# Performance work log

Measured on AMD Instinct MI355X. Metric: run time of the kernel, lower is better.

Reference implementation:

```python
import jax, jax.numpy as jnp
import numpy as np

B, T, C = 2, 2048, 1024
H, DK, OUT = 16, 64, 1024


def setup_inputs() -> dict:
    key = jax.random.key(0)
    k1, k2, k3, k4, k5 = jax.random.split(key, 5)
    glorot_qkv = (2.0 / (C + H * DK)) ** 0.5  # glorot_normal stddev for [C,H,DK]
    glorot_o = (2.0 / (H * DK + OUT)) ** 0.5
    return {
        "x": jax.random.normal(k1, (B, T, C), dtype=jnp.float32),
        "query_mat": jax.random.normal(k2, (C, H, DK), dtype=jnp.float32) * glorot_qkv,
        "key_mat": jax.random.normal(k3, (C, H, DK), dtype=jnp.float32) * glorot_qkv,
        "value_mat": jax.random.normal(k4, (C, H, DK), dtype=jnp.float32) * glorot_qkv,
        "linear_m1": jax.random.normal(k5, (H * DK, OUT), dtype=jnp.float32) * glorot_o,
    }


def reference(x, query_mat, key_mat, value_mat, linear_m1):
    # x: [B,T,C]; projections: [C,H,DK]
    q = jnp.einsum('btc,chd->bhtd', x, query_mat)
    k = jnp.einsum('btc,chd->bhtd', x, key_mat)
    v = jnp.einsum('btc,chd->bhtd', x, value_mat)
    d_k = query_mat.shape[-1]
    # NOTE: faithful to source, which MULTIPLIES by sqrt(d_k)
    w = jnp.einsum('bhtd,bhzd->bhtz', q, k) * (d_k ** 0.5)
    t = w.shape[-1]
    causal = jnp.tril(jnp.ones((t, t), dtype=bool))  # [T,T]
    w = jnp.where(causal, w, -jnp.inf)
    w = jax.nn.softmax(w, axis=-1)
    # dropout inactive (training=False)
    o = jnp.einsum('bhtz,bhzd->bhtd', w, v)
    o = o.transpose(0, 2, 1, 3).reshape(o.shape[0], o.shape[2], -1)  # [B,T,H*DK]
    return jnp.einsum('btc,cz->btz', o, linear_m1)
```

## Files before the change

kernel.cpp:

```cpp
#include <hip/hip_runtime.h>


typedef unsigned short u16;
typedef unsigned int u32;
typedef unsigned long long u64;
typedef __attribute__((ext_vector_type(8))) short bf16x8;
typedef __attribute__((ext_vector_type(4))) float f32x4;

__device__ inline u16 f2bf(float f) {
  union { float f; unsigned u; } v; v.f = f;
  unsigned r = v.u + 0x7FFFu + ((v.u >> 16) & 1u);
  return (u16)(r >> 16);
}
__device__ inline float bf2f(u16 h) {
  union { unsigned u; float f; } v; v.u = ((unsigned)h) << 16;
  return v.f;
}
__device__ inline void glds16(const u16* g, u16* s) {
  __builtin_amdgcn_global_load_lds(
      (const __attribute__((address_space(1))) u32*)g,
      (__attribute__((address_space(3))) u32*)s, 16, 0, 0);
}
#define MFMA __builtin_amdgcn_mfma_f32_16x16x32_bf16
#define SP(P) __builtin_amdgcn_s_setprio(P)

__global__ __launch_bounds__(256) void prep(
    const float* __restrict__ x,
    const float* __restrict__ wq, const float* __restrict__ wk,
    const float* __restrict__ wv, const float* __restrict__ wo,
    u16* __restrict__ Xh, u16* __restrict__ Xl,
    u16* __restrict__ Wqh, u16* __restrict__ Wql,
    u16* __restrict__ Wkh, u16* __restrict__ Wkl,
    u16* __restrict__ Wvt, u16* __restrict__ Wot) {
  const int z = blockIdx.z;
  const int tid = threadIdx.x;
  if (z == 0) {
    const int bid = blockIdx.y * 32 + blockIdx.x;
#pragma unroll
    for (int k = 0; k < 4; k++) {
      int i = bid * 4096 + k * 1024 + tid * 4;
      float4 v = *(const float4*)(x + i);
      ushort4 h, l;
      h.x = f2bf(v.x); l.x = f2bf(v.x - bf2f(h.x));
      h.y = f2bf(v.y); l.y = f2bf(v.y - bf2f(h.y));
      h.z = f2bf(v.z); l.z = f2bf(v.z - bf2f(h.z));
      h.w = f2bf(v.w); l.w = f2bf(v.w - bf2f(h.w));
      *(ushort4*)(Xh + i) = h;
      *(ushort4*)(Xl + i) = l;
    }
    return;
  }
  __shared__ float tile[32][33];
  const float* W = (z == 1) ? wq : (z == 2) ? wk : (z == 3) ? wv : wo;
  const int bx = blockIdx.x * 32, by = blockIdx.y * 32;
  const int tx = tid & 31, ty = tid >> 5;
#pragma unroll
  for (int j = 0; j < 32; j += 8)
    tile[ty + j][tx] = W[(size_t)(by + ty + j) * 1024 + bx + tx];
  __syncthreads();
  if (z <= 2) {
    u16* Th = (z == 1) ? Wqh : Wkh;
    u16* Tl = (z == 1) ? Wql : Wkl;
#pragma unroll
    for (int j = 0; j < 32; j += 8) {
      float v = tile[tx][ty + j];
      u16 h = f2bf(v);
      size_t idx = (size_t)(bx + ty + j) * 1024 + by + tx;
      Th[idx] = h;
      Tl[idx] = f2bf(v - bf2f(h));
    }
  } else {
    u16* T = (z == 3) ? Wvt : Wot;
#pragma unroll
    for (int j = 0; j < 32; j += 8)
      T[(size_t)(bx + ty + j) * 1024 + by + tx] = f2bf(tile[tx][ty + j]);
  }
}

__global__ __launch_bounds__(256) void gemm_qkv(
    const u16* __restrict__ Xh, const u16* __restrict__ Xl,
    const u16* __restrict__ Wqh, const u16* __restrict__ Wql,
    const u16* __restrict__ Wkh, const u16* __restrict__ Wkl,
    const u16* __restrict__ Wvt,
    u16* __restrict__ Qh, u16* __restrict__ Ql,
    u16* __restrict__ Kh, u16* __restrict__ Kl,
    u16* __restrict__ Vt) {
  __shared__ u16 S[4][128][32];
  const int K = 1024;
  const int z = blockIdx.z;
  const bool split = (z < 2);
  const u16* Bh = (z == 0) ? Wqh : (z == 1) ? Wkh : Wvt;
  const u16* Bl = (z == 0) ? Wql : Wkl;
  const int tid = threadIdx.x;
  const int lane = tid & 63, wv = tid >> 6;
  const int quad = lane >> 4, lc = lane & 15;
  const int m0 = (blockIdx.x * 4 + (blockIdx.y & 3)) * 128;
  const int n0 = (blockIdx.y >> 2) * 128;
  const int wm = (wv >> 1) * 64, wn = (wv & 1) * 64;
  const int lrow = lane >> 2, lk = (lane & 3) * 8;
  const u16* a0p = Xh + (size_t)(m0 + wv * 32 + lrow) * K + lk;
  const u16* a1p = a0p + 16 * K;
  const u16* al0p = Xl + (size_t)(m0 + wv * 32 + lrow) * K + lk;
  const u16* al1p = al0p + 16 * K;
  const u16* b0p = Bh + (size_t)(n0 + wv * 32 + lrow) * K + lk;
  const u16* b1p = b0p + 16 * K;
  const u16* bl0p = split ? (Bl + (size_t)(n0 + wv * 32 + lrow) * K + lk) : b0p;
  const u16* bl1p = bl0p + 16 * K;
  u16* sA0 = &S[0][wv * 32][0];      u16* sA1 = &S[0][wv * 32 + 16][0];
  u16* sAl0 = &S[1][wv * 32][0];     u16* sAl1 = &S[1][wv * 32 + 16][0];
  u16* sB0 = &S[2][wv * 32][0];      u16* sB1 = &S[2][wv * 32 + 16][0];
  u16* sBl0 = &S[3][wv * 32][0];     u16* sBl1 = &S[3][wv * 32 + 16][0];
  f32x4 acc[4][4];
#pragma unroll
  for (int i = 0; i < 4; i++)
#pragma unroll
    for (int j = 0; j < 4; j++) acc[i][j] = (f32x4){0.f, 0.f, 0.f, 0.f};
  for (int kc = 0; kc < K; kc += 32) {
    __syncthreads();
    glds16(a0p + kc, sA0); glds16(a1p + kc, sA1);
    glds16(b0p + kc, sB0); glds16(b1p + kc, sB1);
    if (split) {
      glds16(al0p + kc, sAl0); glds16(al1p + kc, sAl1);
      glds16(bl0p + kc, sBl0); glds16(bl1p + kc, sBl1);
    }
    __syncthreads();
    bf16x8 ah[4], al[4];
#pragma unroll
    for (int mt = 0; mt < 4; mt++)
      ah[mt] = *(const bf16x8*)&S[0][wm + mt * 16 + lc][quad * 8];
    if (split) {
#pragma unroll
      for (int mt = 0; mt < 4; mt++)
        al[mt] = *(const bf16x8*)&S[1][wm + mt * 16 + lc][quad * 8];
    }
#pragma unroll
    for (int nt = 0; nt < 4; nt++) {
      bf16x8 bfh = *(const bf16x8*)&S[2][wn + nt * 16 + lc][quad * 8];
#pragma unroll
      for (int mt = 0; mt < 4; mt++)
        acc[mt][nt] = MFMA(ah[mt], bfh, acc[mt][nt], 0, 0, 0);
      if (split) {
        bf16x8 bfl = *(const bf16x8*)&S[3][wn + nt * 16 + lc][quad * 8];
#pragma unroll
        for (int mt = 0; mt < 4; mt++) {
          acc[mt][nt] = MFMA(ah[mt], bfl, acc[mt][nt], 0, 0, 0);
          acc[mt][nt] = MFMA(al[mt], bfh, acc[mt][nt], 0, 0, 0);
        }
      }
    }
  }
  const int rb = quad * 4;
  if (z == 2) {
#pragma unroll
    for (int mt = 0; mt < 4; mt++)
#pragma unroll
      for (int nt = 0; nt < 4; nt++)
#pragma unroll
        for (int r = 0; r < 4; r++) {
          int m = m0 + wm + mt * 16 + rb + r, n = n0 + wn + nt * 16 + lc;
          int b = m >> 11, t = m & 2047, h = n >> 6, d = n & 63;
          Vt[((size_t)(b * 16 + h) * 64 + d) * 2048 + t] = f2bf(acc[mt][nt][r]);
        }
  } else {
    u16* Ch = (z == 0) ? Qh : Kh;
    u16* Cl = (z == 0) ? Ql : Kl;
    const float scale = (z == 0) ? 11.541560327111707f : 1.0f;
#pragma unroll
    for (int mt = 0; mt < 4; mt++)
#pragma unroll
      for (int nt = 0; nt < 4; nt++)
#pragma unroll
        for (int r = 0; r < 4; r++) {
          int m = m0 + wm + mt * 16 + rb + r, n = n0 + wn + nt * 16 + lc;
          int b = m >> 11, t = m & 2047, h = n >> 6, d = n & 63;
          float v = acc[mt][nt][r] * scale;
          u16 hv = f2bf(v);
          size_t idx = ((size_t)(b * 16 + h) * 2048 + t) * 64 + d;
          Ch[idx] = hv;
          Cl[idx] = f2bf(v - bf2f(hv));
        }
  }
}

__global__ __launch_bounds__(256) void gemm_out(const u16* __restrict__ A,
                                                const u16* __restrict__ Bt,
                                                float* __restrict__ C) {
  __shared__ u16 Sa[64][32], Sb[128][32];
  const int K = 1024, N = 1024;
  const int tid = threadIdx.x;
  const int lane = tid & 63, wv = tid >> 6;
  const int quad = lane >> 4, lc = lane & 15;
  const int m0 = (blockIdx.x * 8 + (blockIdx.y & 7)) * 64;
  const int n0 = (blockIdx.y >> 3) * 128;
  const int wm = (wv >> 1) * 32, wn = (wv & 1) * 64;
  const int lrow = lane >> 2, lk = (lane & 3) * 8;
  const u16* ap = A + (size_t)(m0 + wv * 16 + lrow) * K + lk;
  const u16* b0p = Bt + (size_t)(n0 + wv * 32 + lrow) * K + lk;
  const u16* b1p = b0p + 16 * K;
  u16* sA = &Sa[wv * 16][0];
  u16* sB0 = &Sb[wv * 32][0];
  u16* sB1 = &Sb[wv * 32 + 16][0];
  f32x4 acc[2][4];
#pragma unroll
  for (int i = 0; i < 2; i++)
#pragma unroll
    for (int j = 0; j < 4; j++) acc[i][j] = (f32x4){0.f, 0.f, 0.f, 0.f};
  for (int kc = 0; kc < K; kc += 32) {
    __syncthreads();
    glds16(ap + kc, sA);
    glds16(b0p + kc, sB0);
    glds16(b1p + kc, sB1);
    __syncthreads();
    bf16x8 ah[2];
#pragma unroll
    for (int mt = 0; mt < 2; mt++)
      ah[mt] = *(const bf16x8*)&Sa[wm + mt * 16 + lc][quad * 8];
#pragma unroll
    for (int nt = 0; nt < 4; nt++) {
      bf16x8 bfh = *(const bf16x8*)&Sb[wn + nt * 16 + lc][quad * 8];
#pragma unroll
      for (int mt = 0; mt < 2; mt++)
        acc[mt][nt] = MFMA(ah[mt], bfh, acc[mt][nt], 0, 0, 0);
    }
  }
#pragma unroll
  for (int mt = 0; mt < 2; mt++)
#pragma unroll
    for (int nt = 0; nt < 4; nt++)
#pragma unroll
      for (int r = 0; r < 4; r++)
        C[(size_t)(m0 + wm + mt * 16 + quad * 4 + r) * N + n0 + wn + nt * 16 + lc] =
            acc[mt][nt][r];
}

__global__ __launch_bounds__(256, 2) void attn(const u16* __restrict__ Qh,
                                               const u16* __restrict__ Ql,
                                               const u16* __restrict__ Kh,
                                               const u16* __restrict__ Kl,
                                               const u16* __restrict__ Vt,
                                               u16* __restrict__ O16) {
  __shared__ u16 Khs[2][64][64], Kls[2][64][64], Vs[2][64][64];
  __shared__ u16 Ps[4][16][72];
  const int tid = threadIdx.x;
  const int lane = tid & 63, w = tid >> 6;
  const int quad = lane >> 4, lc = lane & 15;
  const int i = blockIdx.x;
  const int bh = i & 31;
  const int qb = 31 - (i >> 5);
  const int ng = qb + 1;
  const int tq = qb * 64 + w * 16 + lc;
  const size_t kbase = (size_t)bh * 2048 * 64;
  const size_t vbase = (size_t)bh * 64 * 2048;
  const size_t qoff = kbase + (size_t)tq * 64 + quad * 8;
  bf16x8 qh0 = *(const bf16x8*)(Qh + qoff);
  bf16x8 qh1 = *(const bf16x8*)(Qh + qoff + 32);
  bf16x8 ql0 = *(const bf16x8*)(Ql + qoff);
  bf16x8 ql1 = *(const bf16x8*)(Ql + qoff + 32);
  const int srow = lane >> 3;
  const int scol = (lane & 7) ^ srow;
  const u16* kg0 = Kh + kbase + (size_t)(w * 16 + srow) * 64 + scol * 8;
  const u16* lg0 = Kl + kbase + (size_t)(w * 16 + srow) * 64 + scol * 8;
  const u16* vg0 = Vt + vbase + (size_t)(w * 16 + srow) * 2048 + scol * 8;

  float mi = -3.0e38f, li = 0.f;
  f32x4 o[4];
#pragma unroll
  for (int d = 0; d < 4; d++) o[d] = (f32x4){0.f, 0.f, 0.f, 0.f};
  const int rx = lc & 7;

  {
    glds16(kg0, &Khs[0][w * 16][0]); glds16(kg0 + 8 * 64, &Khs[0][w * 16 + 8][0]);
    glds16(lg0, &Kls[0][w * 16][0]); glds16(lg0 + 8 * 64, &Kls[0][w * 16 + 8][0]);
    glds16(vg0, &Vs[0][w * 16][0]);  glds16(vg0 + 8 * 2048, &Vs[0][w * 16 + 8][0]);
  }
  for (int g = 0; g < ng; g++) {
    const int buf = g & 1;
    const int z0 = g * 64;
    __syncthreads();
    if (g + 1 < ng) {
      const int zn = (g + 1) * 64;
      const int nb = buf ^ 1;
      glds16(kg0 + (size_t)zn * 64, &Khs[nb][w * 16][0]);
      glds16(kg0 + (size_t)zn * 64 + 8 * 64, &Khs[nb][w * 16 + 8][0]);
      glds16(lg0 + (size_t)zn * 64, &Kls[nb][w * 16][0]);
      glds16(lg0 + (size_t)zn * 64 + 8 * 64, &Kls[nb][w * 16 + 8][0]);
      glds16(vg0 + zn, &Vs[nb][w * 16][0]);
      glds16(vg0 + zn + 8 * 2048, &Vs[nb][w * 16 + 8][0]);
    }
    f32x4 s[4];
    SP(1);
#pragma unroll
    for (int tt = 0; tt < 4; tt++) {
      const int R = tt * 16 + lc;
      bf16x8 kh0 = *(const bf16x8*)&Khs[buf][R][(quad ^ rx) * 8];
      bf16x8 kh1 = *(const bf16x8*)&Khs[buf][R][((4 + quad) ^ rx) * 8];
      bf16x8 kl0 = *(const bf16x8*)&Kls[buf][R][(quad ^ rx) * 8];
      bf16x8 kl1 = *(const bf16x8*)&Kls[buf][R][((4 + quad) ^ rx) * 8];
      f32x4 sv = (f32x4){0.f, 0.f, 0.f, 0.f};
      sv = MFMA(kh0, qh0, sv, 0, 0, 0);
      sv = MFMA(kh1, qh1, sv, 0, 0, 0);
      sv = MFMA(kh0, ql0, sv, 0, 0, 0);
      sv = MFMA(kh1, ql1, sv, 0, 0, 0);
      sv = MFMA(kl0, qh0, sv, 0, 0, 0);
      sv = MFMA(kl1, qh1, sv, 0, 0, 0);
      s[tt] = sv;
    }
    SP(0);
    if (g == ng - 1) {
#pragma unroll
      for (int tt = 0; tt < 4; tt++)
#pragma unroll
        for (int r = 0; r < 4; r++)
          if (z0 + tt * 16 + quad * 4 + r > tq) s[tt][r] = -3.0e38f;
    }
    float smax = -3.0e38f;
#pragma unroll
    for (int tt = 0; tt < 4; tt++)
#pragma unroll
      for (int r = 0; r < 4; r++) smax = fmaxf(smax, s[tt][r]);
    smax = fmaxf(smax, __shfl_xor(smax, 16));
    smax = fmaxf(smax, __shfl_xor(smax, 32));
    if (!__all(smax - mi <= 8.0f)) {
      float mnew = fmaxf(mi, smax);
      float alpha = __builtin_amdgcn_exp2f(mi - mnew);
      mi = mnew;
      li *= alpha;
#pragma unroll
      for (int d = 0; d < 4; d++) o[d] *= alpha;
    }
    float rs = 0.f;
#pragma unroll
    for (int tt = 0; tt < 4; tt++) {
      union { u16 h[4]; u64 d; } pk;
#pragma unroll
      for (int r = 0; r < 4; r++) {
        float p = __builtin_amdgcn_exp2f(s[tt][r] - mi);
        rs += p;
        pk.h[r] = f2bf(p);
      }
      *(u64*)&Ps[w][lc][tt * 16 + quad * 4] = pk.d;
    }
    li += rs;
    bf16x8 pf0 = *(const bf16x8*)&Ps[w][lc][quad * 8];
    bf16x8 pf1 = *(const bf16x8*)&Ps[w][lc][32 + quad * 8];
    SP(1);
#pragma unroll
    for (int dd = 0; dd < 4; dd++) {
      const int R = dd * 16 + lc;
      bf16x8 va0 = *(const bf16x8*)&Vs[buf][R][(quad ^ rx) * 8];
      bf16x8 va1 = *(const bf16x8*)&Vs[buf][R][((4 + quad) ^ rx) * 8];
      o[dd] = MFMA(va0, pf0, o[dd], 0, 0, 0);
      o[dd] = MFMA(va1, pf1, o[dd], 0, 0, 0);
    }
    SP(0);
  }
  li += __shfl_xor(li, 16);
  li += __shfl_xor(li, 32);
  const float rli = 1.0f / li;
  const int b = bh >> 4, hh = bh & 15;
  const size_t obase = ((size_t)(b * 2048 + tq)) * 1024 + hh * 64 + quad * 4;
#pragma unroll
  for (int dd = 0; dd < 4; dd++) {
    ushort4 ov;
    ov.x = f2bf(o[dd][0] * rli);
    ov.y = f2bf(o[dd][1] * rli);
    ov.z = f2bf(o[dd][2] * rli);
    ov.w = f2bf(o[dd][3] * rli);
    *(ushort4*)&O16[obase + dd * 16] = ov;
  }
}

extern "C" void kernel_launch(void* const* d_in, const int* in_sizes, int n_in,
                              void* d_out, int out_size, void* d_ws, size_t ws_size,
                              hipStream_t stream) {
  const float* x  = (const float*)d_in[0];
  const float* wq = (const float*)d_in[1];
  const float* wk = (const float*)d_in[2];
  const float* wv = (const float*)d_in[3];
  const float* wo = (const float*)d_in[4];

  char* w = (char*)d_ws;
  const size_t MB = 1u << 20;
  u16* Xh  = (u16*)(w + 0 * MB);
  u16* Xl  = (u16*)(w + 8 * MB);
  u16* Wqh = (u16*)(w + 16 * MB);
  u16* Wql = (u16*)(w + 18 * MB);
  u16* Wkh = (u16*)(w + 20 * MB);
  u16* Wkl = (u16*)(w + 22 * MB);
  u16* Wvt = (u16*)(w + 24 * MB);
  u16* Wot = (u16*)(w + 26 * MB);
  u16* Qhb = (u16*)(w + 28 * MB);
  u16* Qlb = (u16*)(w + 36 * MB);
  u16* Khb = (u16*)(w + 44 * MB);
  u16* Klb = (u16*)(w + 52 * MB);
  u16* Vtb = (u16*)(w + 60 * MB);
  u16* O16 = (u16*)(w + 0 * MB);

  hipLaunchKernelGGL(prep, dim3(32, 32, 5), dim3(256), 0, stream,
                     x, wq, wk, wv, wo, Xh, Xl, Wqh, Wql, Wkh, Wkl, Wvt, Wot);

  hipLaunchKernelGGL(gemm_qkv, dim3(8, 32, 3), dim3(256), 0, stream,
                     Xh, Xl, Wqh, Wql, Wkh, Wkl, Wvt, Qhb, Qlb, Khb, Klb, Vtb);

  hipLaunchKernelGGL(attn, dim3(1024), dim3(256), 0, stream,
                     Qhb, Qlb, Khb, Klb, Vtb, O16);

  hipLaunchKernelGGL(gemm_out, dim3(8, 64), dim3(256), 0, stream, O16, Wot, (float*)d_out);
}
```

Measured before the change: 214.5 us.

## Load K low-part directly to registers, drop its LDS buffer, raise occupancy

```diff
diff --git a/kernel.cpp b/kernel.cpp
--- a/kernel.cpp
+++ b/kernel.cpp
@@ -233,13 +233,13 @@
             acc[mt][nt][r];
 }
 
-__global__ __launch_bounds__(256, 2) void attn(const u16* __restrict__ Qh,
+__global__ __launch_bounds__(256, 3) void attn(const u16* __restrict__ Qh,
                                                const u16* __restrict__ Ql,
                                                const u16* __restrict__ Kh,
                                                const u16* __restrict__ Kl,
                                                const u16* __restrict__ Vt,
                                                u16* __restrict__ O16) {
-  __shared__ u16 Khs[2][64][64], Kls[2][64][64], Vs[2][64][64];
+  __shared__ u16 Khs[2][64][64], Vs[2][64][64];
   __shared__ u16 Ps[4][16][72];
   const int tid = threadIdx.x;
   const int lane = tid & 63, w = tid >> 6;
@@ -259,8 +259,8 @@
   const int srow = lane >> 3;
   const int scol = (lane & 7) ^ srow;
   const u16* kg0 = Kh + kbase + (size_t)(w * 16 + srow) * 64 + scol * 8;
-  const u16* lg0 = Kl + kbase + (size_t)(w * 16 + srow) * 64 + scol * 8;
   const u16* vg0 = Vt + vbase + (size_t)(w * 16 + srow) * 2048 + scol * 8;
+  const u16* klp = Kl + kbase + (size_t)lc * 64 + quad * 8;
 
   float mi = -3.0e38f, li = 0.f;
   f32x4 o[4];
@@ -268,92 +268,93 @@
   for (int d = 0; d < 4; d++) o[d] = (f32x4){0.f, 0.f, 0.f, 0.f};
   const int rx = lc & 7;
 
-  {
-    glds16(kg0, &Khs[0][w * 16][0]); glds16(kg0 + 8 * 64, &Khs[0][w * 16 + 8][0]);
-    glds16(lg0, &Kls[0][w * 16][0]); glds16(lg0 + 8 * 64, &Kls[0][w * 16 + 8][0]);
-    glds16(vg0, &Vs[0][w * 16][0]);  glds16(vg0 + 8 * 2048, &Vs[0][w * 16 + 8][0]);
-  }
-  for (int g = 0; g < ng; g++) {
-    const int buf = g & 1;
-    const int z0 = g * 64;
-    __syncthreads();
-    if (g + 1 < ng) {
-      const int zn = (g + 1) * 64;
-      const int nb = buf ^ 1;
-      glds16(kg0 + (size_t)zn * 64, &Khs[nb][w * 16][0]);
-      glds16(kg0 + (size_t)zn * 64 + 8 * 64, &Khs[nb][w * 16 + 8][0]);
-      glds16(lg0 + (size_t)zn * 64, &Kls[nb][w * 16][0]);
-      glds16(lg0 + (size_t)zn * 64 + 8 * 64, &Kls[nb][w * 16 + 8][0]);
-      glds16(vg0 + zn, &Vs[nb][w * 16][0]);
-      glds16(vg0 + zn + 8 * 2048, &Vs[nb][w * 16 + 8][0]);
-    }
-    f32x4 s[4];
-    SP(1);
-#pragma unroll
-    for (int tt = 0; tt < 4; tt++) {
-      const int R = tt * 16 + lc;
-      bf16x8 kh0 = *(const bf16x8*)&Khs[buf][R][(quad ^ rx) * 8];
-      bf16x8 kh1 = *(const bf16x8*)&Khs[buf][R][((4 + quad) ^ rx) * 8];
-      bf16x8 kl0 = *(const bf16x8*)&Kls[buf][R][(quad ^ rx) * 8];
-      bf16x8 kl1 = *(const bf16x8*)&Kls[buf][R][((4 + quad) ^ rx) * 8];
-      f32x4 sv = (f32x4){0.f, 0.f, 0.f, 0.f};
-      sv = MFMA(kh0, qh0, sv, 0, 0, 0);
-      sv = MFMA(kh1, qh1, sv, 0, 0, 0);
-      sv = MFMA(kh0, ql0, sv, 0, 0, 0);
-      sv = MFMA(kh1, ql1, sv, 0, 0, 0);
-      sv = MFMA(kl0, qh0, sv, 0, 0, 0);
-      sv = MFMA(kl1, qh1, sv, 0, 0, 0);
-      s[tt] = sv;
-    }
-    SP(0);
-    if (g == ng - 1) {
-#pragma unroll
-      for (int tt = 0; tt < 4; tt++)
-#pragma unroll
-        for (int r = 0; r < 4; r++)
-          if (z0 + tt * 16 + quad * 4 + r > tq) s[tt][r] = -3.0e38f;
-    }
-    float smax = -3.0e38f;
-#pragma unroll
-    for (int tt = 0; tt < 4; tt++)
-#pragma unroll
-      for (int r = 0; r < 4; r++) smax = fmaxf(smax, s[tt][r]);
-    smax = fmaxf(smax, __shfl_xor(smax, 16));
-    smax = fmaxf(smax, __shfl_xor(smax, 32));
-    if (!__all(smax - mi <= 8.0f)) {
-      float mnew = fmaxf(mi, smax);
-      float alpha = __builtin_amdgcn_exp2f(mi - mnew);
-      mi = mnew;
-      li *= alpha;
-#pragma unroll
-      for (int d = 0; d < 4; d++) o[d] *= alpha;
-    }
-    float rs = 0.f;
-#pragma unroll
-    for (int tt = 0; tt < 4; tt++) {
-      union { u16 h[4]; u64 d; } pk;
-#pragma unroll
-      for (int r = 0; r < 4; r++) {
-        float p = __builtin_amdgcn_exp2f(s[tt][r] - mi);
-        rs += p;
-        pk.h[r] = f2bf(p);
-      }
-      *(u64*)&Ps[w][lc][tt * 16 + quad * 4] = pk.d;
-    }
-    li += rs;
-    bf16x8 pf0 = *(const bf16x8*)&Ps[w][lc][quad * 8];
-    bf16x8 pf1 = *(const bf16x8*)&Ps[w][lc][32 + quad * 8];
-    SP(1);
-#pragma unroll
-    for (int dd = 0; dd < 4; dd++) {
-      const int R = dd * 16 + lc;
-      bf16x8 va0 = *(const bf16x8*)&Vs[buf][R][(quad ^ rx) * 8];
-      bf16x8 va1 = *(const bf16x8*)&Vs[buf][R][((4 + quad) ^ rx) * 8];
-      o[dd] = MFMA(va0, pf0, o[dd], 0, 0, 0);
-      o[dd] = MFMA(va1, pf1, o[dd], 0, 0, 0);
-    }
-    SP(0);
-  }
+  bf16x8 kA0[4], kA1[4], kB0[4], kB1[4];
+#define LOAD_KL(D0, D1, G) do { const u16* kg_ = klp + (size_t)(G) * 4096; \
+    _Pragma("unroll") for (int tt = 0; tt < 4; tt++) { \
+      D0[tt] = *(const bf16x8*)(kg_ + tt * 1024); \
+      D1[tt] = *(const bf16x8*)(kg_ + tt * 1024 + 32); } } while (0)
+
+  glds16(kg0, &Khs[0][w * 16][0]); glds16(kg0 + 8 * 64, &Khs[0][w * 16 + 8][0]);
+  glds16(vg0, &Vs[0][w * 16][0]);  glds16(vg0 + 8 * 2048, &Vs[0][w * 16 + 8][0]);
+  LOAD_KL(kA0, kA1, 0);
+
+#define BODY(G, CUR0, CUR1, NXT0, NXT1) do { \
+    const int buf = (G) & 1; \
+    const int z0 = (G) * 64; \
+    __syncthreads();  \
+    if ((G) + 1 < ng) { \
+      const int zn = ((G) + 1) * 64; \
+      const int nb = buf ^ 1; \
+      glds16(kg0 + (size_t)zn * 64, &Khs[nb][w * 16][0]); \
+      glds16(kg0 + (size_t)zn * 64 + 8 * 64, &Khs[nb][w * 16 + 8][0]); \
+      glds16(vg0 + zn, &Vs[nb][w * 16][0]); \
+      glds16(vg0 + zn + 8 * 2048, &Vs[nb][w * 16 + 8][0]); \
+      LOAD_KL(NXT0, NXT1, (G) + 1); \
+    } \
+    f32x4 s[4]; \
+    SP(1); \
+    _Pragma("unroll") for (int tt = 0; tt < 4; tt++) { \
+      const int R = tt * 16 + lc; \
+      bf16x8 kh0 = *(const bf16x8*)&Khs[buf][R][(quad ^ rx) * 8]; \
+      bf16x8 kh1 = *(const bf16x8*)&Khs[buf][R][((4 + quad) ^ rx) * 8]; \
+      f32x4 sv = (f32x4){0.f, 0.f, 0.f, 0.f}; \
+      sv = MFMA(kh0, qh0, sv, 0, 0, 0); \
+      sv = MFMA(kh1, qh1, sv, 0, 0, 0); \
+      sv = MFMA(kh0, ql0, sv, 0, 0, 0); \
+      sv = MFMA(kh1, ql1, sv, 0, 0, 0); \
+      sv = MFMA(CUR0[tt], qh0, sv, 0, 0, 0); \
+      sv = MFMA(CUR1[tt], qh1, sv, 0, 0, 0); \
+      s[tt] = sv; \
+    } \
+    SP(0); \
+    if ((G) == ng - 1) { \
+      _Pragma("unroll") for (int tt = 0; tt < 4; tt++) \
+        _Pragma("unroll") for (int r = 0; r < 4; r++) \
+          if (z0 + tt * 16 + quad * 4 + r > tq) s[tt][r] = -3.0e38f; \
+    } \
+    float smax = -3.0e38f; \
+    _Pragma("unroll") for (int tt = 0; tt < 4; tt++) \
+      _Pragma("unroll") for (int r = 0; r < 4; r++) smax = fmaxf(smax, s[tt][r]); \
+    smax = fmaxf(smax, __shfl_xor(smax, 16)); \
+    smax = fmaxf(smax, __shfl_xor(smax, 32)); \
+    if (!__all(smax - mi <= 8.0f)) { \
+      float mnew = fmaxf(mi, smax); \
+      float alpha = __builtin_amdgcn_exp2f(mi - mnew); \
+      mi = mnew; \
+      li *= alpha; \
+      _Pragma("unroll") for (int d = 0; d < 4; d++) o[d] *= alpha; \
+    } \
+    float rs = 0.f; \
+    _Pragma("unroll") for (int tt = 0; tt < 4; tt++) { \
+      union { u16 h[4]; u64 d; } pk; \
+      _Pragma("unroll") for (int r = 0; r < 4; r++) { \
+        float p = __builtin_amdgcn_exp2f(s[tt][r] - mi); \
+        rs += p; \
+        pk.h[r] = f2bf(p); \
+      } \
+      *(u64*)&Ps[w][lc][tt * 16 + quad * 4] = pk.d; \
+    } \
+    li += rs; \
+    bf16x8 pf0 = *(const bf16x8*)&Ps[w][lc][quad * 8]; \
+    bf16x8 pf1 = *(const bf16x8*)&Ps[w][lc][32 + quad * 8]; \
+    SP(1); \
+    _Pragma("unroll") for (int dd = 0; dd < 4; dd++) { \
+      const int R = dd * 16 + lc; \
+      bf16x8 va0 = *(const bf16x8*)&Vs[buf][R][(quad ^ rx) * 8]; \
+      bf16x8 va1 = *(const bf16x8*)&Vs[buf][R][((4 + quad) ^ rx) * 8]; \
+      o[dd] = MFMA(va0, pf0, o[dd], 0, 0, 0); \
+      o[dd] = MFMA(va1, pf1, o[dd], 0, 0, 0); \
+    } \
+    SP(0); \
+  } while (0)
+
+  for (int g = 0; g < ng; g += 2) {
+    BODY(g, kA0, kA1, kB0, kB1);
+    if (g + 1 < ng) BODY(g + 1, kB0, kB1, kA0, kA1);
+  }
+#undef BODY
+#undef LOAD_KL
+
   li += __shfl_xor(li, 16);
   li += __shfl_xor(li, 32);
   const float rli = 1.0f / li;
```

Measured after the change: 241.9 us. 12.8% more time.

## Double-buffer output GEMM LDS tiles with 64-wide K steps and prefetch

Applied to the files above, without the earlier changes.

```diff
diff --git a/kernel.cpp b/kernel.cpp
--- a/kernel.cpp
+++ b/kernel.cpp
@@ -185,7 +185,7 @@
 __global__ __launch_bounds__(256) void gemm_out(const u16* __restrict__ A,
                                                 const u16* __restrict__ Bt,
                                                 float* __restrict__ C) {
-  __shared__ u16 Sa[64][32], Sb[128][32];
+  __shared__ u16 Sa[2][64][64], Sb[2][128][64];
   const int K = 1024, N = 1024;
   const int tid = threadIdx.x;
   const int lane = tid & 63, wv = tid >> 6;
@@ -193,36 +193,51 @@
   const int m0 = (blockIdx.x * 8 + (blockIdx.y & 7)) * 64;
   const int n0 = (blockIdx.y >> 3) * 128;
   const int wm = (wv >> 1) * 32, wn = (wv & 1) * 64;
-  const int lrow = lane >> 2, lk = (lane & 3) * 8;
-  const u16* ap = A + (size_t)(m0 + wv * 16 + lrow) * K + lk;
-  const u16* b0p = Bt + (size_t)(n0 + wv * 32 + lrow) * K + lk;
-  const u16* b1p = b0p + 16 * K;
-  u16* sA = &Sa[wv * 16][0];
-  u16* sB0 = &Sb[wv * 32][0];
-  u16* sB1 = &Sb[wv * 32 + 16][0];
+  const int srow = lane >> 3, sck = (lane & 7) * 8;
+  const u16* ap = A + (size_t)(m0 + wv * 16 + srow) * K + sck;
+  const u16* bp = Bt + (size_t)(n0 + wv * 32 + srow) * K + sck;
   f32x4 acc[2][4];
 #pragma unroll
   for (int i = 0; i < 2; i++)
 #pragma unroll
     for (int j = 0; j < 4; j++) acc[i][j] = (f32x4){0.f, 0.f, 0.f, 0.f};
-  for (int kc = 0; kc < K; kc += 32) {
+#define STAGE_OUT(KT, BUF) do { \
+    const u16* a_ = ap + (KT) * 64; \
+    glds16(a_, &Sa[BUF][wv * 16][0]); \
+    glds16(a_ + 8 * K, &Sa[BUF][wv * 16 + 8][0]); \
+    const u16* b_ = bp + (KT) * 64; \
+    glds16(b_, &Sb[BUF][wv * 32][0]); \
+    glds16(b_ + 8 * K, &Sb[BUF][wv * 32 + 8][0]); \
+    glds16(b_ + 16 * K, &Sb[BUF][wv * 32 + 16][0]); \
+    glds16(b_ + 24 * K, &Sb[BUF][wv * 32 + 24][0]); \
+  } while (0)
+  STAGE_OUT(0, 0);
+  for (int kt = 0; kt < 16; kt++) {
+    const int buf = kt & 1;
     __syncthreads();
-    glds16(ap + kc, sA);
-    glds16(b0p + kc, sB0);
-    glds16(b1p + kc, sB1);
-    __syncthreads();
-    bf16x8 ah[2];
+    if (kt + 1 < 16) STAGE_OUT(kt + 1, buf ^ 1);
+    bf16x8 afr[2][2], bfr[4][2];
 #pragma unroll
     for (int mt = 0; mt < 2; mt++)
-      ah[mt] = *(const bf16x8*)&Sa[wm + mt * 16 + lc][quad * 8];
-#pragma unroll
-    for (int nt = 0; nt < 4; nt++) {
-      bf16x8 bfh = *(const bf16x8*)&Sb[wn + nt * 16 + lc][quad * 8];
+#pragma unroll
+      for (int ks = 0; ks < 2; ks++)
+        afr[mt][ks] = *(const bf16x8*)&Sa[buf][wm + mt * 16 + lc][quad * 8 + ks * 32];
+#pragma unroll
+    for (int nt = 0; nt < 4; nt++)
+#pragma unroll
+      for (int ks = 0; ks < 2; ks++)
+        bfr[nt][ks] = *(const bf16x8*)&Sb[buf][wn + nt * 16 + lc][quad * 8 + ks * 32];
+    SP(1);
+#pragma unroll
+    for (int nt = 0; nt < 4; nt++)
 #pragma unroll
       for (int mt = 0; mt < 2; mt++)
-        acc[mt][nt] = MFMA(ah[mt], bfh, acc[mt][nt], 0, 0, 0);
-    }
-  }
+#pragma unroll
+        for (int ks = 0; ks < 2; ks++)
+          acc[mt][nt] = MFMA(afr[mt][ks], bfr[nt][ks], acc[mt][nt], 0, 0, 0);
+    SP(0);
+  }
+#undef STAGE_OUT
 #pragma unroll
   for (int mt = 0; mt < 2; mt++)
 #pragma unroll
```

New measurement: 216.6 us. Within noise of the previous version (+1.0%).
